# Kernel tuning notes

Hardware: AMD Instinct MI355X
Metric: run time of the kernel (lower is better)

The kernel has to match this reference:

```python
import jax, jax.numpy as jnp
import numpy as np

B, L, D, H = 2, 2048, 1024, 16
HD = D // H  # head dim = 64


def setup_inputs() -> dict:
    key = jax.random.key(0)
    ks = jax.random.split(key, 5)
    s = 1.0 / np.sqrt(D)
    return {
        "x": jax.random.normal(ks[0], (B, L, D), dtype=jnp.float32),
        "mask": jnp.ones((B, 1, 1, L), dtype=jnp.int32),
        "Wq": jax.random.normal(ks[1], (D, D), dtype=jnp.float32) * s,
        "bq": jnp.zeros((D,), dtype=jnp.float32),
        "Wk": jax.random.normal(ks[2], (D, D), dtype=jnp.float32) * s,
        "bk": jnp.zeros((D,), dtype=jnp.float32),
        "Wv": jax.random.normal(ks[3], (D, D), dtype=jnp.float32) * s,
        "bv": jnp.zeros((D,), dtype=jnp.float32),
        "Wo": jax.random.normal(ks[4], (D, D), dtype=jnp.float32) * s,
        "bo": jnp.zeros((D,), dtype=jnp.float32),
    }


def reference(x, mask, Wq, bq, Wk, bk, Wv, bv, Wo, bo):
    Bx, Lx = x.shape[0], x.shape[1]
    # torch nn.Linear: y = x @ W.T + b
    q = (jnp.einsum("bld,ed->ble", x, Wq) + bq).reshape(Bx, Lx, H, HD).transpose(0, 2, 1, 3)
    k = (jnp.einsum("bld,ed->ble", x, Wk) + bk).reshape(Bx, Lx, H, HD).transpose(0, 2, 1, 3)
    v = (jnp.einsum("bld,ed->ble", x, Wv) + bv).reshape(Bx, Lx, H, HD).transpose(0, 2, 1, 3)
    # [B, H, L, L] scores
    scores = jnp.einsum("bhqd,bhkd->bhqk", q, k) / np.sqrt(HD).astype(np.float32)
    # faithful to original: masked positions are set to the tiny value 1e-9 (not -inf)
    scores = jnp.where(mask == 0, jnp.float32(1e-9), scores)
    attn = jax.nn.softmax(scores, axis=-1)
    # dropout_prob=0.0 -> identity (eval mode)
    out = jnp.einsum("bhqk,bhkd->bhqd", attn, v)  # [B, H, L, HD]
    out = out.transpose(0, 2, 1, 3).reshape(Bx, Lx, D)
    return jnp.einsum("bld,ed->ble", out, Wo) + bo
```

## Files before the change

kernel.cpp:

```cpp
#include <hip/hip_runtime.h>
#include <hip/hip_bf16.h>

typedef _Float16 f16;
typedef _Float16 f16x8 __attribute__((ext_vector_type(8)));
typedef _Float16 f16x4 __attribute__((ext_vector_type(4)));
typedef float f32x4 __attribute__((ext_vector_type(4)));
typedef int i32x4 __attribute__((ext_vector_type(4)));

#define LDS_LOAD16(gptr, lptr)                                                             \
  __builtin_amdgcn_global_load_lds(                                                        \
      (const __attribute__((address_space(1))) unsigned int*)(gptr),                       \
      (__attribute__((address_space(3))) unsigned int*)(lptr), 16, 0, 0)

#define ALPHA 0.18033688f
#define MASKVAL 1.44269504e-9f

__global__ __launch_bounds__(256) void conv_all(const float* __restrict__ x,
                                                const float* __restrict__ Wq,
                                                const float* __restrict__ Wk,
                                                const float* __restrict__ Wv,
                                                const float* __restrict__ Wo,
                                                f16* __restrict__ xh, f16* __restrict__ wqh,
                                                f16* __restrict__ wkh, f16* __restrict__ wvh,
                                                f16* __restrict__ woh) {
  int i = blockIdx.x * 256 + threadIdx.x;
  const float* src;
  f16* dst;
  int off;
  if (i < 524288) {
    src = x; dst = xh; off = i;
  } else {
    int j = i - 524288;
    int w = j >> 17;
    off = j & 131071;
    src = (w == 0) ? Wq : (w == 1) ? Wk : (w == 2) ? Wv : Wo;
    dst = (w == 0) ? wqh : (w == 1) ? wkh : (w == 2) ? wvh : woh;
  }
  const float4* s4 = (const float4*)src;
  float4 a = s4[2 * off];
  float4 b = s4[2 * off + 1];
  f16x8 o = {(f16)a.x, (f16)a.y, (f16)a.z, (f16)a.w,
             (f16)b.x, (f16)b.y, (f16)b.z, (f16)b.w};
  *(f16x8*)(dst + (size_t)off * 8) = o;
}

__global__ __launch_bounds__(256) void gemm_qkv(const f16* __restrict__ A,
                                                const f16* __restrict__ W0,
                                                const f16* __restrict__ W1,
                                                const f16* __restrict__ W2,
                                                const float* __restrict__ b0,
                                                const float* __restrict__ b1,
                                                const float* __restrict__ b2,
                                                f16* __restrict__ qo, f16* __restrict__ ko,
                                                f16* __restrict__ vo) {
  constexpr int K = 1024, BM = 128, BK = 32, NKT = K / BK;
  __shared__ f16 aT[2][BM * BK];
  __shared__ f16 bT[2][BM * BK];
  const int z = blockIdx.z;
  const f16* Bw = (z == 0) ? W0 : (z == 1) ? W1 : W2;
  const float* bias = (z == 0) ? b0 : (z == 1) ? b1 : b2;
  const int tid = threadIdx.x, wid = tid >> 6, lane = tid & 63;
  const int mb = blockIdx.y * BM, nb = blockIdx.x * BM;
  const int wr = wid >> 1, wc = wid & 1;
  const int lr = lane & 15, hi = lane >> 4;

  f32x4 acc[4][4] = {};

  const int r0 = tid >> 2, s0 = tid & 3;
  const int ci1 = 256 + tid, r1 = ci1 >> 2, s1 = ci1 & 3;

#define STAGE_QKV(bb, kt)                                                                   \
  do {                                                                                      \
    const int kb_ = (kt) * BK;                                                              \
    LDS_LOAD16(A + (size_t)(mb + r0) * K + kb_ + s0 * 8, (char*)aT[bb] + wid * 1024);       \
    LDS_LOAD16(Bw + (size_t)(nb + r0) * K + kb_ + s0 * 8, (char*)bT[bb] + wid * 1024);      \
    LDS_LOAD16(A + (size_t)(mb + r1) * K + kb_ + s1 * 8, (char*)aT[bb] + 4096 + wid * 1024);\
    LDS_LOAD16(Bw + (size_t)(nb + r1) * K + kb_ + s1 * 8, (char*)bT[bb] + 4096 + wid * 1024);\
  } while (0)

  STAGE_QKV(0, 0);
  for (int kt = 0; kt < NKT; ++kt) {
    const int p = kt & 1;
    if (kt + 1 < NKT) {
      STAGE_QKV(p ^ 1, kt + 1);
      asm volatile("s_waitcnt vmcnt(4)" ::: "memory");
    } else {
      asm volatile("s_waitcnt vmcnt(0)" ::: "memory");
    }
    __builtin_amdgcn_s_barrier();

    f16x8 af[4], bf[4];
#pragma unroll
    for (int i = 0; i < 4; ++i) af[i] = *(const f16x8*)&aT[p][(wr * 64 + i * 16 + lr) * BK + hi * 8];
#pragma unroll
    for (int j = 0; j < 4; ++j) bf[j] = *(const f16x8*)&bT[p][(wc * 64 + j * 16 + lr) * BK + hi * 8];
    __builtin_amdgcn_s_setprio(1);
#pragma unroll
    for (int i = 0; i < 4; ++i)
#pragma unroll
      for (int j = 0; j < 4; ++j)
        acc[i][j] = __builtin_amdgcn_mfma_f32_16x16x32_f16(af[i], bf[j], acc[i][j], 0, 0, 0);
    __builtin_amdgcn_s_setprio(0);
    __builtin_amdgcn_s_barrier();
  }

  const float scale = (z == 0) ? ALPHA : 1.0f;
#pragma unroll
  for (int i = 0; i < 4; ++i) {
#pragma unroll
    for (int j = 0; j < 4; ++j) {
      const int row = mb + wr * 64 + i * 16 + hi * 4;
      const int col = nb + wc * 64 + j * 16 + lr;
      const float bv = bias[col];
      const int hh = col >> 6, dd = col & 63;
      if (z == 2) {
        const int bb = row >> 11, l = row & 2047;
        f16x4 v4;
#pragma unroll
        for (int r = 0; r < 4; ++r) v4[r] = (f16)(acc[i][j][r] + bv);
        *(f16x4*)(vo + ((((size_t)bb * 16 + hh) * 64 + dd) * 2048 + l)) = v4;
      } else {
        f16* o = z ? ko : qo;
#pragma unroll
        for (int r = 0; r < 4; ++r) {
          const int m2 = row + r;
          const int bb = m2 >> 11, l = m2 & 2047;
          o[((((size_t)bb * 16 + hh) * 2048 + l) * 64) + dd] = (f16)((acc[i][j][r] + bv) * scale);
        }
      }
    }
  }
}

__global__ __launch_bounds__(256) void gemm_o(const f16* __restrict__ A,
                                              const f16* __restrict__ W,
                                              const float* __restrict__ bias,
                                              float* __restrict__ out) {
  constexpr int K = 1024, N = 1024, BK = 32, NKT = K / BK;
  __shared__ f16 aT[2][64 * BK];
  __shared__ f16 bT[2][128 * BK];
  const int tid = threadIdx.x, wid = tid >> 6, lane = tid & 63;
  const int lr = lane & 15, hi = lane >> 4;
  const int mb = blockIdx.y * 64, nb = blockIdx.x * 128;
  const int wr = wid >> 1, wc = wid & 1;
  f32x4 acc[2][4] = {};
  const int ra = tid >> 2, sa = tid & 3;
  const int rb1 = (256 + tid) >> 2, sb1 = (256 + tid) & 3;

#define STAGE_O(bb, kt)                                                                     \
  do {                                                                                      \
    const int kb_ = (kt) * BK;                                                              \
    LDS_LOAD16(A + (size_t)(mb + ra) * K + kb_ + sa * 8, (char*)aT[bb] + wid * 1024);       \
    LDS_LOAD16(W + (size_t)(nb + ra) * K + kb_ + sa * 8, (char*)bT[bb] + wid * 1024);       \
    LDS_LOAD16(W + (size_t)(nb + rb1) * K + kb_ + sb1 * 8, (char*)bT[bb] + 4096 + wid * 1024);\
  } while (0)

  STAGE_O(0, 0);
  for (int kt = 0; kt < NKT; ++kt) {
    const int p = kt & 1;
    if (kt + 1 < NKT) {
      STAGE_O(p ^ 1, kt + 1);
      asm volatile("s_waitcnt vmcnt(3)" ::: "memory");
    } else {
      asm volatile("s_waitcnt vmcnt(0)" ::: "memory");
    }
    __builtin_amdgcn_s_barrier();
    f16x8 af[2], bf[4];
#pragma unroll
    for (int i = 0; i < 2; ++i) af[i] = *(const f16x8*)&aT[p][(wr * 32 + i * 16 + lr) * BK + hi * 8];
#pragma unroll
    for (int j = 0; j < 4; ++j) bf[j] = *(const f16x8*)&bT[p][(wc * 64 + j * 16 + lr) * BK + hi * 8];
    __builtin_amdgcn_s_setprio(1);
#pragma unroll
    for (int i = 0; i < 2; ++i)
#pragma unroll
      for (int j = 0; j < 4; ++j)
        acc[i][j] = __builtin_amdgcn_mfma_f32_16x16x32_f16(af[i], bf[j], acc[i][j], 0, 0, 0);
    __builtin_amdgcn_s_setprio(0);
    __builtin_amdgcn_s_barrier();
  }
#pragma unroll
  for (int i = 0; i < 2; ++i)
#pragma unroll
    for (int j = 0; j < 4; ++j) {
      const int col = nb + wc * 64 + j * 16 + lr;
      const float bv = bias[col];
#pragma unroll
      for (int r = 0; r < 4; ++r)
        out[(size_t)(mb + wr * 32 + i * 16 + hi * 4 + r) * N + col] = acc[i][j][r] + bv;
    }
}

__global__ __launch_bounds__(128, 2) void attn2w(const f16* __restrict__ Qh,
                                                 const f16* __restrict__ Kh,
                                                 const f16* __restrict__ Vt,
                                                 const int* __restrict__ mask,
                                                 f16* __restrict__ Oa) {
  constexpr int L = 2048, HD = 64, H = 16, NT = L / 64;
  __shared__ __align__(16) char ldsb[32768];

  const int tid = threadIdx.x, w = tid >> 6, lane = tid & 63;
  const int lr = lane & 15, hi = lane >> 4;
  const int sw = lr & 7;
  const bool oddhi = (hi & 1) != 0;

  const int bid = blockIdx.x;
  const int head = (bid & 7) * 4 + (bid >> 8);
  const int qb = (bid >> 3) & 31;
  const int b = head >> 4, h = head & 15;
  const int qr0 = qb * 64 + w * 32;

  const f16* Qb = Qh + (size_t)head * L * HD;
  const f16* Kb = Kh + (size_t)head * L * HD;
  const f16* Vb = Vt + (size_t)head * HD * L;
  const int* mrow = mask + b * L;

  int mred = 1;
  {
    const int4* m4 = (const int4*)mrow;
#pragma unroll
    for (int j = 0; j < 8; ++j) {
      int4 v = m4[lane + j * 64];
      mred &= v.x & v.y & v.z & v.w;
    }
  }
  const bool allm = __all(mred == 1);

  const int srow = lane >> 3;
  const int schk = (lane & 7) ^ srow;

#define STAGE2W(bb, kt)                                                                     \
  _Pragma("unroll") for (int c = 0; c < 4; ++c) {                                           \
    LDS_LOAD16(Kb + (size_t)((kt) * 64 + w * 32 + c * 8 + srow) * HD + schk * 8,            \
               ldsb + (bb) * 16384 + w * 4096 + c * 1024);                                  \
    LDS_LOAD16(Vb + (size_t)(w * 32 + c * 8 + srow) * L + (kt) * 64 + schk * 8,             \
               ldsb + (bb) * 16384 + 8192 + w * 4096 + c * 1024);                           \
  }

  const char* kbase0 = ldsb + lr * 128 + ((hi ^ sw) * 16);
  const char* kbase1 = ldsb + lr * 128 + (((4 + hi) ^ sw) * 16);

  f16x8 qf[2][2];
#pragma unroll
  for (int qg = 0; qg < 2; ++qg)
#pragma unroll
    for (int k2 = 0; k2 < 2; ++k2)
      qf[qg][k2] = *(const f16x8*)&Qb[(size_t)(qr0 + qg * 16 + lr) * HD + k2 * 32 + hi * 8];

  f32x4 oacc[2][4] = {};
  f32x4 lacc[2] = {};
  const f32x4 zacc = {0.f, 0.f, 0.f, 0.f};
  const f16x8 ones = {1, 1, 1, 1, 1, 1, 1, 1};

  int4 mvA[4], mvB[4];
  if (!allm) {
#pragma unroll
    for (int nf = 0; nf < 4; ++nf) mvA[nf] = *(const int4*)&mrow[nf * 16 + hi * 4];
  }
  STAGE2W(0, 0);

#define ATTN_ITER(kt, P, MVR, MVL)                                                          \
  do {                                                                                      \
    asm volatile("s_waitcnt vmcnt(0)" ::: "memory");                                        \
    __builtin_amdgcn_s_barrier();                                                           \
    if ((kt) + 1 < NT) {                                                                    \
      if (!allm) {                                                                          \
        _Pragma("unroll") for (int nf = 0; nf < 4; ++nf)                                    \
            MVL[nf] = *(const int4*)&mrow[((kt) + 1) * 64 + nf * 16 + hi * 4];              \
      }                                                                                     \
      STAGE2W((P) ^ 1, (kt) + 1);                                                           \
    }                                                                                       \
    f16x8 kf[4][2];                                                                         \
    _Pragma("unroll") for (int nf = 0; nf < 4; ++nf) {                                      \
      kf[nf][0] = *(const f16x8*)(kbase0 + (P) * 16384 + nf * 2048);                        \
      kf[nf][1] = *(const f16x8*)(kbase1 + (P) * 16384 + nf * 2048);                        \
    }                                                                                       \
    f32x4 s[2][4];                                                                          \
    __builtin_amdgcn_s_setprio(1);                                                          \
    _Pragma("unroll") for (int qg = 0; qg < 2; ++qg)                                        \
        _Pragma("unroll") for (int nf = 0; nf < 4; ++nf) {                                  \
      f32x4 z = __builtin_amdgcn_mfma_f32_16x16x32_f16(kf[nf][0], qf[qg][0], zacc, 0, 0, 0);\
      s[qg][nf] = __builtin_amdgcn_mfma_f32_16x16x32_f16(kf[nf][1], qf[qg][1], z, 0, 0, 0); \
    }                                                                                       \
    __builtin_amdgcn_s_setprio(0);                                                          \
    f16x8 pf[2][2];                                                                         \
    _Pragma("unroll") for (int qg = 0; qg < 2; ++qg) {                                      \
      int wpk[4][2];                                                                        \
      _Pragma("unroll") for (int nf = 0; nf < 4; ++nf) {                                    \
        float p0, p1, p2, p3;                                                               \
        if (allm) {                                                                         \
          p0 = __builtin_amdgcn_exp2f(s[qg][nf][0]);                                        \
          p1 = __builtin_amdgcn_exp2f(s[qg][nf][1]);                                        \
          p2 = __builtin_amdgcn_exp2f(s[qg][nf][2]);                                        \
          p3 = __builtin_amdgcn_exp2f(s[qg][nf][3]);                                        \
        } else {                                                                            \
          p0 = __builtin_amdgcn_exp2f(MVR[nf].x ? s[qg][nf][0] : MASKVAL);                  \
          p1 = __builtin_amdgcn_exp2f(MVR[nf].y ? s[qg][nf][1] : MASKVAL);                  \
          p2 = __builtin_amdgcn_exp2f(MVR[nf].z ? s[qg][nf][2] : MASKVAL);                  \
          p3 = __builtin_amdgcn_exp2f(MVR[nf].w ? s[qg][nf][3] : MASKVAL);                  \
        }                                                                                   \
        wpk[nf][0] = __builtin_bit_cast(int, __builtin_amdgcn_cvt_pkrtz(p0, p1));           \
        wpk[nf][1] = __builtin_bit_cast(int, __builtin_amdgcn_cvt_pkrtz(p2, p3));           \
      }                                                                                     \
      _Pragma("unroll") for (int k2 = 0; k2 < 2; ++k2) {                                    \
        int A0 = wpk[2 * k2][0], B0 = wpk[2 * k2 + 1][0];                                   \
        int A1 = wpk[2 * k2][1], B1 = wpk[2 * k2 + 1][1];                                   \
        asm("v_permlane32_swap_b32 %0, %1" : "+v"(A0), "+v"(B0));                           \
        asm("v_permlane32_swap_b32 %0, %1" : "+v"(A1), "+v"(B1));                           \
        int SA0 = __builtin_amdgcn_ds_swizzle(A0, 0x401F);                                  \
        int SB0 = __builtin_amdgcn_ds_swizzle(B0, 0x401F);                                  \
        int SA1 = __builtin_amdgcn_ds_swizzle(A1, 0x401F);                                  \
        int SB1 = __builtin_amdgcn_ds_swizzle(B1, 0x401F);                                  \
        int c0 = oddhi ? SB0 : A0;                                                          \
        int c1 = oddhi ? SB1 : A1;                                                          \
        int c2 = oddhi ? B0 : SA0;                                                          \
        int c3 = oddhi ? B1 : SA1;                                                          \
        i32x4 cc = {c0, c1, c2, c3};                                                        \
        pf[qg][k2] = __builtin_bit_cast(f16x8, cc);                                         \
      }                                                                                     \
    }                                                                                       \
    __builtin_amdgcn_s_setprio(1);                                                          \
    _Pragma("unroll") for (int k2 = 0; k2 < 2; ++k2) {                                      \
      const char* vbase = (k2 ? kbase1 : kbase0) + (P) * 16384 + 8192;                      \
      _Pragma("unroll") for (int df = 0; df < 4; ++df) {                                    \
        f16x8 vf = *(const f16x8*)(vbase + df * 2048);                                      \
        oacc[0][df] = __builtin_amdgcn_mfma_f32_16x16x32_f16(pf[0][k2], vf, oacc[0][df], 0, 0, 0); \
        oacc[1][df] = __builtin_amdgcn_mfma_f32_16x16x32_f16(pf[1][k2], vf, oacc[1][df], 0, 0, 0); \
      }                                                                                     \
      lacc[0] = __builtin_amdgcn_mfma_f32_16x16x32_f16(pf[0][k2], ones, lacc[0], 0, 0, 0);  \
      lacc[1] = __builtin_amdgcn_mfma_f32_16x16x32_f16(pf[1][k2], ones, lacc[1], 0, 0, 0);  \
    }                                                                                       \
    __builtin_amdgcn_s_setprio(0);                                                          \
  } while (0)

  for (int kt = 0; kt < NT; kt += 2) {
    ATTN_ITER(kt, 0, mvA, mvB);
    ATTN_ITER(kt + 1, 1, mvB, mvA);
  }

#pragma unroll
  for (int qg = 0; qg < 2; ++qg) {
    f32x4 rinv;
#pragma unroll
    for (int r = 0; r < 4; ++r) rinv[r] = 1.0f / lacc[qg][r];
#pragma unroll
    for (int df = 0; df < 4; ++df)
#pragma unroll
      for (int r = 0; r < 4; ++r) {
        const int l = qr0 + qg * 16 + hi * 4 + r;
        Oa[(((size_t)b * L + l) * H + h) * HD + df * 16 + lr] = (f16)(oacc[qg][df][r] * rinv[r]);
      }
  }
}

extern "C" void kernel_launch(void* const* d_in, const int* in_sizes, int n_in,
                              void* d_out, int out_size, void* d_ws, size_t ws_size,
                              hipStream_t stream) {
  const float* x  = (const float*)d_in[0];
  const int* mask = (const int*)d_in[1];
  const float* Wq = (const float*)d_in[2];
  const float* bq = (const float*)d_in[3];
  const float* Wk = (const float*)d_in[4];
  const float* bk = (const float*)d_in[5];
  const float* Wv = (const float*)d_in[6];
  const float* bv = (const float*)d_in[7];
  const float* Wo = (const float*)d_in[8];
  const float* bo = (const float*)d_in[9];
  float* out = (float*)d_out;

  char* ws = (char*)d_ws;
  const size_t MB = 1u << 20;
  f16* xh  = (f16*)(ws);
  f16* wqh = (f16*)(ws + 8 * MB);
  f16* wkh = (f16*)(ws + 10 * MB);
  f16* wvh = (f16*)(ws + 12 * MB);
  f16* woh = (f16*)(ws + 14 * MB);
  f16* qh  = (f16*)(ws + 16 * MB);
  f16* kh  = (f16*)(ws + 24 * MB);
  f16* vth = (f16*)(ws + 32 * MB);
  f16* oah = (f16*)(ws + 40 * MB);

  conv_all<<<4096, 256, 0, stream>>>(x, Wq, Wk, Wv, Wo, xh, wqh, wkh, wvh, woh);

  gemm_qkv<<<dim3(8, 32, 3), 256, 0, stream>>>(xh, wqh, wkh, wvh, bq, bk, bv, qh, kh, vth);

  attn2w<<<dim3(1024), 128, 0, stream>>>(qh, kh, vth, mask, oah);

  gemm_o<<<dim3(8, 64), 256, 0, stream>>>(oah, woh, bo, out);
}
```

Measured before the change: 119.7 us.

## Split attention query block across four waves of 16 rows each

The attention kernel goes from 2 waves with 32 query rows each to 4 waves with 16 query rows each per 64-row block. The K/V staging into LDS is spread across the four waves. The intent is more wavefronts per CU, to hide latency and lower per-thread register pressure. In exchange, each K/V fragment read from LDS is reused over fewer query rows, so LDS read traffic per MFMA roughly doubles.

```diff
diff --git a/kernel.cpp b/kernel.cpp
--- a/kernel.cpp
+++ b/kernel.cpp
@@ -191,7 +191,7 @@
     }
 }
 
-__global__ __launch_bounds__(128, 2) void attn2w(const f16* __restrict__ Qh,
+__global__ __launch_bounds__(256, 4) void attn4w(const f16* __restrict__ Qh,
                                                  const f16* __restrict__ Kh,
                                                  const f16* __restrict__ Vt,
                                                  const int* __restrict__ mask,
@@ -208,7 +208,7 @@
   const int head = (bid & 7) * 4 + (bid >> 8);
   const int qb = (bid >> 3) & 31;
   const int b = head >> 4, h = head & 15;
-  const int qr0 = qb * 64 + w * 32;
+  const int qr0 = qb * 64 + w * 16;
 
   const f16* Qb = Qh + (size_t)head * L * HD;
   const f16* Kb = Kh + (size_t)head * L * HD;
@@ -229,26 +229,24 @@
   const int srow = lane >> 3;
   const int schk = (lane & 7) ^ srow;
 
-#define STAGE2W(bb, kt)                                                                     \
-  _Pragma("unroll") for (int c = 0; c < 4; ++c) {                                           \
-    LDS_LOAD16(Kb + (size_t)((kt) * 64 + w * 32 + c * 8 + srow) * HD + schk * 8,            \
-               ldsb + (bb) * 16384 + w * 4096 + c * 1024);                                  \
-    LDS_LOAD16(Vb + (size_t)(w * 32 + c * 8 + srow) * L + (kt) * 64 + schk * 8,             \
-               ldsb + (bb) * 16384 + 8192 + w * 4096 + c * 1024);                           \
+#define STAGE4W(bb, kt)                                                                     \
+  _Pragma("unroll") for (int c = 0; c < 2; ++c) {                                           \
+    LDS_LOAD16(Kb + (size_t)((kt) * 64 + w * 16 + c * 8 + srow) * HD + schk * 8,            \
+               ldsb + (bb) * 16384 + w * 2048 + c * 1024);                                  \
+    LDS_LOAD16(Vb + (size_t)(w * 16 + c * 8 + srow) * L + (kt) * 64 + schk * 8,             \
+               ldsb + (bb) * 16384 + 8192 + w * 2048 + c * 1024);                           \
   }
 
   const char* kbase0 = ldsb + lr * 128 + ((hi ^ sw) * 16);
   const char* kbase1 = ldsb + lr * 128 + (((4 + hi) ^ sw) * 16);
 
-  f16x8 qf[2][2];
-#pragma unroll
-  for (int qg = 0; qg < 2; ++qg)
-#pragma unroll
-    for (int k2 = 0; k2 < 2; ++k2)
-      qf[qg][k2] = *(const f16x8*)&Qb[(size_t)(qr0 + qg * 16 + lr) * HD + k2 * 32 + hi * 8];
-
-  f32x4 oacc[2][4] = {};
-  f32x4 lacc[2] = {};
+  f16x8 qf[2];
+#pragma unroll
+  for (int k2 = 0; k2 < 2; ++k2)
+    qf[k2] = *(const f16x8*)&Qb[(size_t)(qr0 + lr) * HD + k2 * 32 + hi * 8];
+
+  f32x4 oacc[4] = {};
+  f32x4 lacc = {};
   const f32x4 zacc = {0.f, 0.f, 0.f, 0.f};
   const f16x8 ones = {1, 1, 1, 1, 1, 1, 1, 1};
 
@@ -257,7 +255,7 @@
 #pragma unroll
     for (int nf = 0; nf < 4; ++nf) mvA[nf] = *(const int4*)&mrow[nf * 16 + hi * 4];
   }
-  STAGE2W(0, 0);
+  STAGE4W(0, 0);
 
 #define ATTN_ITER(kt, P, MVR, MVL)                                                          \
   do {                                                                                      \
@@ -268,67 +266,62 @@
         _Pragma("unroll") for (int nf = 0; nf < 4; ++nf)                                    \
             MVL[nf] = *(const int4*)&mrow[((kt) + 1) * 64 + nf * 16 + hi * 4];              \
       }                                                                                     \
-      STAGE2W((P) ^ 1, (kt) + 1);                                                           \
+      STAGE4W((P) ^ 1, (kt) + 1);                                                           \
     }                                                                                       \
     f16x8 kf[4][2];                                                                         \
     _Pragma("unroll") for (int nf = 0; nf < 4; ++nf) {                                      \
       kf[nf][0] = *(const f16x8*)(kbase0 + (P) * 16384 + nf * 2048);                        \
       kf[nf][1] = *(const f16x8*)(kbase1 + (P) * 16384 + nf * 2048);                        \
     }                                                                                       \
-    f32x4 s[2][4];                                                                          \
+    f32x4 s[4];                                                                             \
     __builtin_amdgcn_s_setprio(1);                                                          \
-    _Pragma("unroll") for (int qg = 0; qg < 2; ++qg)                                        \
-        _Pragma("unroll") for (int nf = 0; nf < 4; ++nf) {                                  \
-      f32x4 z = __builtin_amdgcn_mfma_f32_16x16x32_f16(kf[nf][0], qf[qg][0], zacc, 0, 0, 0);\
-      s[qg][nf] = __builtin_amdgcn_mfma_f32_16x16x32_f16(kf[nf][1], qf[qg][1], z, 0, 0, 0); \
+    _Pragma("unroll") for (int nf = 0; nf < 4; ++nf) {                                      \
+      f32x4 z = __builtin_amdgcn_mfma_f32_16x16x32_f16(kf[nf][0], qf[0], zacc, 0, 0, 0);    \
+      s[nf] = __builtin_amdgcn_mfma_f32_16x16x32_f16(kf[nf][1], qf[1], z, 0, 0, 0);         \
     }                                                                                       \
     __builtin_amdgcn_s_setprio(0);                                                          \
-    f16x8 pf[2][2];                                                                         \
-    _Pragma("unroll") for (int qg = 0; qg < 2; ++qg) {                                      \
-      int wpk[4][2];                                                                        \
-      _Pragma("unroll") for (int nf = 0; nf < 4; ++nf) {                                    \
-        float p0, p1, p2, p3;                                                               \
-        if (allm) {                                                                         \
-          p0 = __builtin_amdgcn_exp2f(s[qg][nf][0]);                                        \
-          p1 = __builtin_amdgcn_exp2f(s[qg][nf][1]);                                        \
-          p2 = __builtin_amdgcn_exp2f(s[qg][nf][2]);                                        \
-          p3 = __builtin_amdgcn_exp2f(s[qg][nf][3]);                                        \
-        } else {                                                                            \
-          p0 = __builtin_amdgcn_exp2f(MVR[nf].x ? s[qg][nf][0] : MASKVAL);                  \
-          p1 = __builtin_amdgcn_exp2f(MVR[nf].y ? s[qg][nf][1] : MASKVAL);                  \
-          p2 = __builtin_amdgcn_exp2f(MVR[nf].z ? s[qg][nf][2] : MASKVAL);                  \
-          p3 = __builtin_amdgcn_exp2f(MVR[nf].w ? s[qg][nf][3] : MASKVAL);                  \
-        }                                                                                   \
-        wpk[nf][0] = __builtin_bit_cast(int, __builtin_amdgcn_cvt_pkrtz(p0, p1));           \
-        wpk[nf][1] = __builtin_bit_cast(int, __builtin_amdgcn_cvt_pkrtz(p2, p3));           \
+    int wpk[4][2];                                                                          \
+    _Pragma("unroll") for (int nf = 0; nf < 4; ++nf) {                                      \
+      float p0, p1, p2, p3;                                                                 \
+      if (allm) {                                                                           \
+        p0 = __builtin_amdgcn_exp2f(s[nf][0]);                                              \
+        p1 = __builtin_amdgcn_exp2f(s[nf][1]);                                              \
+        p2 = __builtin_amdgcn_exp2f(s[nf][2]);                                              \
+        p3 = __builtin_amdgcn_exp2f(s[nf][3]);                                              \
+      } else {                                                                              \
+        p0 = __builtin_amdgcn_exp2f(MVR[nf].x ? s[nf][0] : MASKVAL);                        \
+        p1 = __builtin_amdgcn_exp2f(MVR[nf].y ? s[nf][1] : MASKVAL);                        \
+        p2 = __builtin_amdgcn_exp2f(MVR[nf].z ? s[nf][2] : MASKVAL);                        \
+        p3 = __builtin_amdgcn_exp2f(MVR[nf].w ? s[nf][3] : MASKVAL);                        \
       }                                                                                     \
-      _Pragma("unroll") for (int k2 = 0; k2 < 2; ++k2) {                                    \
-        int A0 = wpk[2 * k2][0], B0 = wpk[2 * k2 + 1][0];                                   \
-        int A1 = wpk[2 * k2][1], B1 = wpk[2 * k2 + 1][1];                                   \
-        asm("v_permlane32_swap_b32 %0, %1" : "+v"(A0), "+v"(B0));                           \
-        asm("v_permlane32_swap_b32 %0, %1" : "+v"(A1), "+v"(B1));                           \
-        int SA0 = __builtin_amdgcn_ds_swizzle(A0, 0x401F);                                  \
-        int SB0 = __builtin_amdgcn_ds_swizzle(B0, 0x401F);                                  \
-        int SA1 = __builtin_amdgcn_ds_swizzle(A1, 0x401F);                                  \
-        int SB1 = __builtin_amdgcn_ds_swizzle(B1, 0x401F);                                  \
-        int c0 = oddhi ? SB0 : A0;                                                          \
-        int c1 = oddhi ? SB1 : A1;                                                          \
-        int c2 = oddhi ? B0 : SA0;                                                          \
-        int c3 = oddhi ? B1 : SA1;                                                          \
-        i32x4 cc = {c0, c1, c2, c3};                                                        \
-        pf[qg][k2] = __builtin_bit_cast(f16x8, cc);                                         \
-      }                                                                                     \
+      wpk[nf][0] = __builtin_bit_cast(int, __builtin_amdgcn_cvt_pkrtz(p0, p1));             \
+      wpk[nf][1] = __builtin_bit_cast(int, __builtin_amdgcn_cvt_pkrtz(p2, p3));             \
+    }                                                                                       \
+    f16x8 pf[2];                                                                            \
+    _Pragma("unroll") for (int k2 = 0; k2 < 2; ++k2) {                                      \
+      int A0 = wpk[2 * k2][0], B0 = wpk[2 * k2 + 1][0];                                     \
+      int A1 = wpk[2 * k2][1], B1 = wpk[2 * k2 + 1][1];                                     \
+      asm("v_permlane32_swap_b32 %0, %1" : "+v"(A0), "+v"(B0));                             \
+      asm("v_permlane32_swap_b32 %0, %1" : "+v"(A1), "+v"(B1));                             \
+      int SA0 = __builtin_amdgcn_ds_swizzle(A0, 0x401F);                                    \
+      int SB0 = __builtin_amdgcn_ds_swizzle(B0, 0x401F);                                    \
+      int SA1 = __builtin_amdgcn_ds_swizzle(A1, 0x401F);                                    \
+      int SB1 = __builtin_amdgcn_ds_swizzle(B1, 0x401F);                                    \
+      int c0 = oddhi ? SB0 : A0;                                                            \
+      int c1 = oddhi ? SB1 : A1;                                                            \
+      int c2 = oddhi ? B0 : SA0;                                                            \
+      int c3 = oddhi ? B1 : SA1;                                                            \
+      i32x4 cc = {c0, c1, c2, c3};                                                          \
+      pf[k2] = __builtin_bit_cast(f16x8, cc);                                               \
     }                                                                                       \
     __builtin_amdgcn_s_setprio(1);                                                          \
     _Pragma("unroll") for (int k2 = 0; k2 < 2; ++k2) {                                      \
       const char* vbase = (k2 ? kbase1 : kbase0) + (P) * 16384 + 8192;                      \
       _Pragma("unroll") for (int df = 0; df < 4; ++df) {                                    \
         f16x8 vf = *(const f16x8*)(vbase + df * 2048);                                      \
-        oacc[0][df] = __builtin_amdgcn_mfma_f32_16x16x32_f16(pf[0][k2], vf, oacc[0][df], 0, 0, 0); \
-        oacc[1][df] = __builtin_amdgcn_mfma_f32_16x16x32_f16(pf[1][k2], vf, oacc[1][df], 0, 0, 0); \
+        oacc[df] = __builtin_amdgcn_mfma_f32_16x16x32_f16(pf[k2], vf, oacc[df], 0, 0, 0);   \
       }                                                                                     \
-      lacc[0] = __builtin_amdgcn_mfma_f32_16x16x32_f16(pf[0][k2], ones, lacc[0], 0, 0, 0);  \
-      lacc[1] = __builtin_amdgcn_mfma_f32_16x16x32_f16(pf[1][k2], ones, lacc[1], 0, 0, 0);  \
+      lacc = __builtin_amdgcn_mfma_f32_16x16x32_f16(pf[k2], ones, lacc, 0, 0, 0);           \
     }                                                                                       \
     __builtin_amdgcn_s_setprio(0);                                                          \
   } while (0)
@@ -338,19 +331,16 @@
     ATTN_ITER(kt + 1, 1, mvB, mvA);
   }
 
-#pragma unroll
-  for (int qg = 0; qg < 2; ++qg) {
-    f32x4 rinv;
-#pragma unroll
-    for (int r = 0; r < 4; ++r) rinv[r] = 1.0f / lacc[qg][r];
-#pragma unroll
-    for (int df = 0; df < 4; ++df)
-#pragma unroll
-      for (int r = 0; r < 4; ++r) {
-        const int l = qr0 + qg * 16 + hi * 4 + r;
-        Oa[(((size_t)b * L + l) * H + h) * HD + df * 16 + lr] = (f16)(oacc[qg][df][r] * rinv[r]);
-      }
-  }
+  f32x4 rinv;
+#pragma unroll
+  for (int r = 0; r < 4; ++r) rinv[r] = 1.0f / lacc[r];
+#pragma unroll
+  for (int df = 0; df < 4; ++df)
+#pragma unroll
+    for (int r = 0; r < 4; ++r) {
+      const int l = qr0 + hi * 4 + r;
+      Oa[(((size_t)b * L + l) * H + h) * HD + df * 16 + lr] = (f16)(oacc[df][r] * rinv[r]);
+    }
 }
 
 extern "C" void kernel_launch(void* const* d_in, const int* in_sizes, int n_in,
@@ -384,7 +374,7 @@
 
   gemm_qkv<<<dim3(8, 32, 3), 256, 0, stream>>>(xh, wqh, wkh, wvh, bq, bk, bv, qh, kh, vth);
 
-  attn2w<<<dim3(1024), 128, 0, stream>>>(qh, kh, vth, mask, oah);
+  attn4w<<<dim3(1024), 256, 0, stream>>>(qh, kh, vth, mask, oah);
 
   gemm_o<<<dim3(8, 64), 256, 0, stream>>>(oah, woh, bo, out);
 }
```

Result: no change. 118.3 us (-1.1%).
